# Performance work log

Hardware: AMD Instinct MI355X
Metric: run time of the kernel (lower is better)

Reference implementation:

```python
import math
import jax, jax.numpy as jnp
import numpy as np

HEAD_NUM = 8
DIM = 512
D_K = DIM // HEAD_NUM  # 64
M_FEAT = 256
B, L = 4, 2048
STAB = 1e-5


def _orthogonal_gaussian(m, d, rng):
    num_squares = m // d
    blocks = []
    for _ in range(num_squares):
        q, _ = np.linalg.qr(rng.standard_normal((d, d)))
        blocks.append(q.T)
    rem = m - d * num_squares
    if rem:
        q, _ = np.linalg.qr(rng.standard_normal((d, d)))
        blocks.append(q.T[:rem])
    mat = np.concatenate(blocks, axis=0)
    mat = mat / math.sqrt(num_squares + rem / d)
    return mat.astype(np.float32)


def setup_inputs() -> dict:
    key = jax.random.key(0)
    ks = jax.random.split(key, 12)
    rng = np.random.default_rng(0)
    inp = {
        'query': jax.random.normal(ks[0], (B, L, DIM), jnp.float32),
        'key': jax.random.normal(ks[1], (B, L, DIM), jnp.float32),
        'value': jax.random.normal(ks[2], (B, L, DIM), jnp.float32),
        'proj': jnp.asarray(_orthogonal_gaussian(M_FEAT, D_K, rng)),  # [M, d_k]
        'w_q_w': jax.random.normal(ks[3], (DIM, DIM), jnp.float32) * 0.02,
        'w_q_b': jnp.zeros((DIM,), jnp.float32),
        'w_k_w': jax.random.normal(ks[4], (DIM, DIM), jnp.float32) * 0.02,
        'w_k_b': jnp.zeros((DIM,), jnp.float32),
        'w_v_w': jax.random.normal(ks[5], (DIM, DIM), jnp.float32) * 0.02,
        'w_v_b': jnp.zeros((DIM,), jnp.float32),
        'w_o_w': jax.random.normal(ks[6], (DIM, DIM), jnp.float32) * 0.02,
        'w_o_b': jnp.zeros((DIM,), jnp.float32),
    }
    return inp


def _relu_kernel(data, proj):
    # data: [B,L,H,D], proj: [M,D] -> [B,L,H,M]
    ratio = 1.0 / math.sqrt(proj.shape[0])
    return jax.nn.relu(ratio * jnp.einsum('blhd,md->blhm', data, proj)) + STAB


def _favor_causal(qp, kp, vs):
    # qp, kp: [L,B,H,M]; vs: [L,B,H,D] -> num [L,B,H,D], den [L,B,H]
    b, h, m = qp.shape[1], qp.shape[2], qp.shape[3]
    d = vs.shape[3]
    carry0 = (jnp.zeros((b, h, m, d), qp.dtype), jnp.zeros((b, h, m), qp.dtype))

    def step(carry, inp):
        s_kv, s_k = carry
        q_l, k_l, v_l = inp
        s_kv = s_kv + jnp.einsum('bhm,bhd->bhmd', k_l, v_l)
        s_k = s_k + k_l
        num = jnp.einsum('bhmd,bhm->bhd', s_kv, q_l)
        den = jnp.sum(q_l * s_k, axis=-1)
        return (s_kv, s_k), (num, den)

    _, (num, den) = jax.lax.scan(step, carry0, (qp, kp, vs))
    return num, den


def reference(query, key, value, proj, w_q_w, w_q_b, w_k_w, w_k_b, w_v_w, w_v_b, w_o_w, w_o_b):
    bsz = query.shape[0]
    q = (query @ w_q_w.T + w_q_b).reshape(bsz, -1, HEAD_NUM, D_K)
    k = (key @ w_k_w.T + w_k_b).reshape(bsz, -1, HEAD_NUM, D_K)
    v = (value @ w_v_w.T + w_v_b).reshape(bsz, -1, HEAD_NUM, D_K)
    qp = jnp.swapaxes(_relu_kernel(q, proj), 0, 1)  # [L,B,H,M]
    kp = jnp.swapaxes(_relu_kernel(k, proj), 0, 1)
    vs = jnp.swapaxes(v, 0, 1)                      # [L,B,H,D]
    num, den = _favor_causal(qp, kp, vs)
    attn = jnp.swapaxes(num, 0, 1) / jnp.swapaxes(den, 0, 1)[..., None]  # [B,L,H,D]
    attn = attn.reshape(bsz, -1, HEAD_NUM * D_K)
    return attn @ w_o_w.T + w_o_b
```

## Files before the change

kernel.cpp:

```cpp
#include <hip/hip_runtime.h>
#include <stdint.h>

#define B_ 4
#define L_ 2048
#define H_ 8
#define DK 64
#define M_ 256
#define DIM_ 512
#define NTOK (B_ * L_)
#define CHK 128
#define NC (L_ / CHK)
#define BH (B_ * H_)
#define RATIO 0.0625f
#define STABC 1e-5f

typedef unsigned short ushort_t;
typedef __attribute__((ext_vector_type(8))) short bf8v;
typedef __attribute__((ext_vector_type(4))) float f4v;

#define MFMA16(a, b, c) __builtin_amdgcn_mfma_f32_16x16x32_bf16(a, b, c, 0, 0, 0)

__device__ __forceinline__ ushort_t f2bf(float f) {
  uint32_t u = __float_as_uint(f);
  return (ushort_t)((u + 0x7fffu + ((u >> 16) & 1u)) >> 16);
}
__device__ __forceinline__ float bf2f(ushort_t u) { return __uint_as_float(((uint32_t)u) << 16); }

__device__ __forceinline__ void gll16(const void* g, void* l) {
  __builtin_amdgcn_global_load_lds((const __attribute__((address_space(1))) void*)g,
                                   (__attribute__((address_space(3))) void*)l, 16, 0, 0);
}

__device__ __forceinline__ bf8v ldfrag(const ushort_t* base, int row, int cb) {
  return *(const bf8v*)((const char*)base + row * 128 + (cb ^ ((row & 7) << 4)));
}
__device__ __forceinline__ bf8v ldfrag256(const ushort_t* base, int row, int cb) {
  return *(const bf8v*)((const char*)base + row * 256 + (cb ^ ((row & 7) << 4)));
}
__device__ __forceinline__ bf8v ldfrag512(const ushort_t* base, int row, int cb) {
  return *(const bf8v*)((const char*)base + row * 512 + (cb ^ ((row & 7) << 4)));
}

__global__ __launch_bounds__(256) void cvt_w(const float* __restrict__ wq, const float* __restrict__ wk,
                                             const float* __restrict__ wv, const float* __restrict__ wo,
                                             const float* __restrict__ pj, ushort_t* __restrict__ d) {
  int i = (blockIdx.x * 256 + threadIdx.x) * 8;
  const float* s;
  int off;
  if (i < 262144)       { s = wq; off = i; }
  else if (i < 524288)  { s = wk; off = i - 262144; }
  else if (i < 786432)  { s = wv; off = i - 524288; }
  else if (i < 1048576) { s = wo; off = i - 786432; }
  else                  { s = pj; off = i - 1048576; }
  float4 a = *(const float4*)(s + off);
  float4 b = *(const float4*)(s + off + 4);
  union { ushort_t u[8]; uint4 vv; } o;
  o.u[0] = f2bf(a.x); o.u[1] = f2bf(a.y); o.u[2] = f2bf(a.z); o.u[3] = f2bf(a.w);
  o.u[4] = f2bf(b.x); o.u[5] = f2bf(b.y); o.u[6] = f2bf(b.z); o.u[7] = f2bf(b.w);
  *(uint4*)(d + i) = o.vv;
}

__global__ __launch_bounds__(256) void qkvgemm_k(const float* __restrict__ q, const float* __restrict__ k,
                                                 const float* __restrict__ v, const ushort_t* __restrict__ Wc,
                                                 const float* __restrict__ bq, const float* __restrict__ bk,
                                                 const float* __restrict__ bv, ushort_t* __restrict__ XHq,
                                                 ushort_t* __restrict__ XHk, ushort_t* __restrict__ VT) {
  __shared__ char SB[34816];
  ushort_t* As = (ushort_t*)SB;
  ushort_t* Bs = (ushort_t*)(SB + 16384);
  ushort_t* Tt = (ushort_t*)SB;
  const int z = blockIdx.z;
  const float* X = (z == 0) ? q : (z == 1) ? k : v;
  const ushort_t* Bw = Wc + (size_t)z * 262144;
  const float* bias = (z == 0) ? bq : (z == 1) ? bk : bv;
  const int tid = threadIdx.x, lane = tid & 63, w = tid >> 6;
  const int bm = blockIdx.x * 128, bn = blockIdx.y * 128;
  const int srow = w * 8 + (lane >> 3);
  const int scol = (((lane & 7) * 16) ^ ((lane >> 3) << 4)) >> 1;
  const int wr = (w >> 1) * 64, wc = (w & 1) * 64;
  const int fr = lane & 15, ks = lane >> 4, fq = lane >> 4;
  f4v acc[4][4] = {};
  for (int k0 = 0; k0 < DIM_; k0 += 64) {
#pragma unroll
    for (int i = 0; i < 4; ++i)
      gll16(Bw + (size_t)(bn + i * 32 + srow) * DIM_ + k0 + scol, (char*)Bs + i * 4096 + w * 1024);
#pragma unroll
    for (int i = 0; i < 4; ++i) {
      int e = tid + i * 256;
      int r = e >> 3, g = e & 7;
      const float* src = X + (size_t)(bm + r) * DIM_ + k0 + g * 8;
      float4 f0 = *(const float4*)src;
      float4 f1 = *(const float4*)(src + 4);
      union { ushort_t u[8]; bf8v v8; } pk;
      pk.u[0] = f2bf(f0.x); pk.u[1] = f2bf(f0.y); pk.u[2] = f2bf(f0.z); pk.u[3] = f2bf(f0.w);
      pk.u[4] = f2bf(f1.x); pk.u[5] = f2bf(f1.y); pk.u[6] = f2bf(f1.z); pk.u[7] = f2bf(f1.w);
      *(bf8v*)((char*)As + r * 128 + ((g * 16) ^ ((r & 7) << 4))) = pk.v8;
    }
    __syncthreads();
#pragma unroll
    for (int kk = 0; kk < 2; ++kk) {
      const int cb = kk * 64 + ks * 16;
      bf8v av[4], bv2[4];
#pragma unroll
      for (int m = 0; m < 4; ++m) av[m] = ldfrag(As, wr + m * 16 + fr, cb);
#pragma unroll
      for (int n = 0; n < 4; ++n) bv2[n] = ldfrag(Bs, wc + n * 16 + fr, cb);
#pragma unroll
      for (int m = 0; m < 4; ++m)
#pragma unroll
        for (int n = 0; n < 4; ++n) acc[m][n] = MFMA16(av[m], bv2[n], acc[m][n]);
    }
    __syncthreads();
  }
  if (z == 2) {
#pragma unroll
    for (int m = 0; m < 4; ++m)
#pragma unroll
      for (int n = 0; n < 4; ++n) {
        int cl = wc + n * 16 + fr;
        float bsv = bias[bn + cl];
#pragma unroll
        for (int j = 0; j < 4; ++j) {
          int rl = wr + m * 16 + fq * 4 + j;
          Tt[cl * 136 + rl] = f2bf(acc[m][n][j] + bsv);
        }
      }
    __syncthreads();
    const int dl = tid >> 1, seg = tid & 1;
    const int c = bn + dl;
    const int bh2 = (bm >> 11) * 8 + (c >> 6);
    const int drow = c & 63;
    size_t vbase = ((size_t)(bh2 * 64 + drow)) * L_ + (bm & 2047) + seg * 64;
#pragma unroll
    for (int qq = 0; qq < 8; ++qq)
      *(uint4*)&VT[vbase + qq * 8] = *(const uint4*)&Tt[dl * 136 + seg * 64 + qq * 8];
  } else {
    ushort_t* Y = (z == 0) ? XHq : XHk;
#pragma unroll
    for (int m = 0; m < 4; ++m)
#pragma unroll
      for (int n = 0; n < 4; ++n) {
        int col = bn + wc + n * 16 + fr;
        float bsv = bias[col];
#pragma unroll
        for (int j = 0; j < 4; ++j) {
          int row = bm + wr + m * 16 + fq * 4 + j;
          Y[(size_t)row * DIM_ + col] = f2bf(acc[m][n][j] + bsv);
        }
      }
  }
}

__global__ __launch_bounds__(256) void cp2_k(const ushort_t* __restrict__ XHk, const ushort_t* __restrict__ P,
                                             const ushort_t* __restrict__ VT, ushort_t* __restrict__ kp,
                                             ushort_t* __restrict__ S) {
  __shared__ ushort_t Ps[256 * 64];
  __shared__ ushort_t Xs[128 * 64];
  __shared__ ushort_t Kt[256 * 128];
  const int ci = blockIdx.x, bh = blockIdx.y;
  const int b = bh >> 3, h = bh & 7;
  const int tid = threadIdx.x, lane = tid & 63, w = tid >> 6;
  const int srow = w * 8 + (lane >> 3);
  const int scol = (((lane & 7) * 16) ^ ((lane >> 3) << 4)) >> 1;
  const int fr = lane & 15, ks = lane >> 4, fq = lane >> 4;
  const int l0 = ci * CHK;
#pragma unroll
  for (int i = 0; i < 8; ++i)
    gll16(P + (size_t)(i * 32 + srow) * 64 + scol, (char*)Ps + i * 4096 + w * 1024);
#pragma unroll
  for (int i = 0; i < 4; ++i)
    gll16(XHk + (size_t)(b * L_ + l0 + i * 32 + srow) * DIM_ + h * 64 + scol, (char*)Xs + i * 4096 + w * 1024);
  __syncthreads();
  {
    f4v acc[4][8] = {};
#pragma unroll
    for (int kk = 0; kk < 2; ++kk) {
      const int cb = kk * 64 + ks * 16;
      bf8v av[4], bv[8];
#pragma unroll
      for (int m = 0; m < 4; ++m) av[m] = ldfrag(Ps, w * 64 + m * 16 + fr, cb);
#pragma unroll
      for (int n = 0; n < 8; ++n) bv[n] = ldfrag(Xs, n * 16 + fr, cb);
#pragma unroll
      for (int m = 0; m < 4; ++m)
#pragma unroll
        for (int n = 0; n < 8; ++n) acc[m][n] = MFMA16(av[m], bv[n], acc[m][n]);
    }
#pragma unroll
    for (int m = 0; m < 4; ++m)
#pragma unroll
      for (int n = 0; n < 8; ++n) {
        const int mb = w * 64 + m * 16 + fq * 4;
        const int ll = n * 16 + fr;
        ushort_t bvv[4];
#pragma unroll
        for (int j = 0; j < 4; ++j) {
          float v = fmaxf(RATIO * acc[m][n][j], 0.f) + STABC;
          bvv[j] = f2bf(v);
          *(ushort_t*)((char*)Kt + (mb + j) * 256 + ((ll * 2) ^ (((mb + j) & 7) << 4))) = bvv[j];
        }
        uint2 pk;
        pk.x = (uint32_t)bvv[0] | ((uint32_t)bvv[1] << 16);
        pk.y = (uint32_t)bvv[2] | ((uint32_t)bvv[3] << 16);
        *(uint2*)(kp + ((size_t)bh * L_ + l0 + ll) * M_ + mb) = pk;
      }
  }
  __syncthreads();
  f4v accS[5][4] = {};
  for (int kt = 0; kt < 2; ++kt) {
#pragma unroll
    for (int i = 0; i < 2; ++i)
      gll16(VT + ((size_t)bh * 64 + i * 32 + srow) * L_ + l0 + kt * 64 + scol, (char*)Xs + i * 4096 + w * 1024);
    if (tid < 32) ((uint32_t*)Xs)[2048 + tid] = 0x3f803f80u;
    __syncthreads();
#pragma unroll
    for (int kk = 0; kk < 2; ++kk) {
      const int cbA = kk * 64 + ks * 16;
      const int cbK = kt * 128 + kk * 64 + ks * 16;
      bf8v av[5], bv[4];
#pragma unroll
      for (int a = 0; a < 5; ++a) av[a] = ldfrag(Xs, a * 16 + fr, cbA);
#pragma unroll
      for (int n = 0; n < 4; ++n) bv[n] = ldfrag256(Kt, w * 64 + n * 16 + fr, cbK);
#pragma unroll
      for (int a = 0; a < 5; ++a)
#pragma unroll
        for (int n = 0; n < 4; ++n) accS[a][n] = MFMA16(av[a], bv[n], accS[a][n]);
    }
    __syncthreads();
  }
  const size_t base = ((size_t)bh * NC + ci) * 65;
#pragma unroll
  for (int a = 0; a < 5; ++a)
#pragma unroll
    for (int n = 0; n < 4; ++n)
#pragma unroll
      for (int j = 0; j < 4; ++j) {
        int row = a * 16 + fq * 4 + j;
        if (row < 65) S[(base + row) * M_ + w * 64 + n * 16 + fr] = f2bf(accS[a][n][j]);
      }
}

__global__ __launch_bounds__(256) void prefix2_k(ushort_t* __restrict__ S) {
  const int g = blockIdx.x * 256 + threadIdx.x;
  const int bh = g / 2080, r = g - bh * 2080;
  ushort_t* base = S + (size_t)bh * (NC * 65 * M_) + (size_t)r * 8;
  uint4 v[16];
#pragma unroll
  for (int ci = 0; ci < NC; ++ci) v[ci] = *(const uint4*)(base + (size_t)ci * (65 * M_));
  float c[8] = {};
#pragma unroll
  for (int ci = 0; ci < NC; ++ci) {
    union { uint4 u; ushort_t s[8]; } in, out;
    in.u = v[ci];
#pragma unroll
    for (int e = 0; e < 8; ++e) {
      float t = bf2f(in.s[e]);
      out.s[e] = f2bf(c[e]);
      c[e] += t;
    }
    *(uint4*)(base + (size_t)ci * (65 * M_)) = out.u;
  }
}

__global__ __launch_bounds__(512) void qkout3_k(const ushort_t* __restrict__ XHq, const ushort_t* __restrict__ P,
                                                const ushort_t* __restrict__ kp, const ushort_t* __restrict__ VT,
                                                const ushort_t* __restrict__ S, ushort_t* __restrict__ attn) {
  __shared__ char LB[114688];
  ushort_t* Qp = (ushort_t*)LB;
  ushort_t* R1 = (ushort_t*)(LB + 65536);
  ushort_t* R2 = (ushort_t*)(LB + 98304);
  const int ci = blockIdx.x, bh = blockIdx.y;
  const int b = bh >> 3, h = bh & 7;
  const int tid = threadIdx.x, lane = tid & 63, w = tid >> 6;
  const int srow = w * 8 + (lane >> 3);
  const int scol = (((lane & 7) * 16) ^ ((lane >> 3) << 4)) >> 1;
  const int fr = lane & 15, ks = lane >> 4, fq = lane >> 4;
  const int l0 = ci * CHK;
  const size_t rowb = (size_t)bh * L_ + l0;
  const size_t tokb = (size_t)b * L_ + l0;
  const size_t sbase = ((size_t)bh * NC + ci) * 65;
#pragma unroll
  for (int i = 0; i < 4; ++i)
    gll16(P + (size_t)(i * 64 + srow) * 64 + scol, (char*)R1 + i * 8192 + w * 1024);
#pragma unroll
  for (int i = 0; i < 2; ++i)
    gll16(XHq + (tokb + i * 64 + srow) * DIM_ + h * 64 + scol, (char*)R2 + i * 8192 + w * 1024);
  __syncthreads();
  {
    f4v accF[2][8] = {};
#pragma unroll
    for (int kk = 0; kk < 2; ++kk) {
      const int cb = kk * 64 + ks * 16;
      bf8v av[2], bv[8];
#pragma unroll
      for (int m = 0; m < 2; ++m) av[m] = ldfrag(R1, w * 32 + m * 16 + fr, cb);
#pragma unroll
      for (int n = 0; n < 8; ++n) bv[n] = ldfrag(R2, n * 16 + fr, cb);
#pragma unroll
      for (int m = 0; m < 2; ++m)
#pragma unroll
        for (int n = 0; n < 8; ++n) accF[m][n] = MFMA16(av[m], bv[n], accF[m][n]);
    }
#pragma unroll
    for (int m = 0; m < 2; ++m)
#pragma unroll
      for (int n = 0; n < 8; ++n) {
        const int mb = w * 32 + m * 16 + fq * 4;
        const int ll = n * 16 + fr;
        ushort_t bvv[4];
#pragma unroll
        for (int j = 0; j < 4; ++j)
          bvv[j] = f2bf(fmaxf(RATIO * accF[m][n][j], 0.f) + STABC);
        uint2 pk;
        pk.x = (uint32_t)bvv[0] | ((uint32_t)bvv[1] << 16);
        pk.y = (uint32_t)bvv[2] | ((uint32_t)bvv[3] << 16);
        *(uint2*)((char*)Qp + ll * 512 + ((mb * 2) ^ ((ll & 7) << 4))) = pk;
      }
  }
  __syncthreads();
  const int qr = (w & 3) * 32, qc = (w >> 2) * 64;
  const int orow = w * 16;
  f4v accA[2][4] = {};
  f4v acc2[5] = {};
  for (int kt = 0; kt < 4; ++kt) {
#pragma unroll
    for (int i = 0; i < 2; ++i)
      gll16(kp + (rowb + i * 64 + srow) * M_ + kt * 64 + scol, (char*)R1 + i * 8192 + w * 1024);
    gll16(S + (sbase + srow) * M_ + kt * 64 + scol, (char*)R2 + w * 1024);
    if (tid < 32)
      ((uint32_t*)R2)[2048 + tid] = ((const uint32_t*)(S + (sbase + 64) * M_ + kt * 64))[tid];
    __syncthreads();
#pragma unroll
    for (int kk = 0; kk < 2; ++kk) {
      const int cb = kk * 64 + ks * 16;
      const int cbQ = kt * 128 + cb;
      bf8v aq[2], bk_[4], a2, sv[5];
#pragma unroll
      for (int m = 0; m < 2; ++m) aq[m] = ldfrag512(Qp, qr + m * 16 + fr, cbQ);
#pragma unroll
      for (int n = 0; n < 4; ++n) bk_[n] = ldfrag(R1, qc + n * 16 + fr, cb);
#pragma unroll
      for (int m = 0; m < 2; ++m)
#pragma unroll
        for (int n = 0; n < 4; ++n) accA[m][n] = MFMA16(aq[m], bk_[n], accA[m][n]);
      a2 = ldfrag512(Qp, orow + fr, cbQ);
#pragma unroll
      for (int n = 0; n < 5; ++n) sv[n] = ldfrag(R2, n * 16 + fr, cb);
#pragma unroll
      for (int n = 0; n < 5; ++n) acc2[n] = MFMA16(a2, sv[n], acc2[n]);
    }
    __syncthreads();
  }
#pragma unroll
  for (int m = 0; m < 2; ++m)
#pragma unroll
    for (int n = 0; n < 4; ++n)
#pragma unroll
      for (int j = 0; j < 4; ++j) {
        int row = qr + m * 16 + fq * 4 + j;
        int col = qc + n * 16 + fr;
        float v = (col <= row) ? accA[m][n][j] : 0.f;
        *(ushort_t*)((char*)R1 + row * 256 + ((col * 2) ^ ((row & 7) << 4))) = f2bf(v);
      }
  __syncthreads();
  for (int kt2 = 0; kt2 < 2; ++kt2) {
    gll16(VT + ((size_t)bh * 64 + srow) * L_ + l0 + kt2 * 64 + scol, (char*)R2 + w * 1024);
    if (tid < 32) ((uint32_t*)R2)[2048 + tid] = 0x3f803f80u;
    __syncthreads();
#pragma unroll
    for (int kk = 0; kk < 2; ++kk) {
      const int cb = kk * 64 + ks * 16;
      bf8v a3, sv[5];
      a3 = ldfrag256(R1, orow + fr, kt2 * 128 + cb);
#pragma unroll
      for (int n = 0; n < 5; ++n) sv[n] = ldfrag(R2, n * 16 + fr, cb);
#pragma unroll
      for (int n = 0; n < 5; ++n) acc2[n] = MFMA16(a3, sv[n], acc2[n]);
    }
    __syncthreads();
  }
  float dinv[4];
#pragma unroll
  for (int j = 0; j < 4; ++j) {
    float den = __shfl(acc2[4][j], (lane & 48));
    dinv[j] = 1.f / den;
  }
#pragma unroll
  for (int n = 0; n < 4; ++n)
#pragma unroll
    for (int j = 0; j < 4; ++j) {
      int l = orow + fq * 4 + j;
      int col = h * 64 + n * 16 + fr;
      attn[(tokb + l) * DIM_ + col] = f2bf(acc2[n][j] * dinv[j]);
    }
}

__global__ __launch_bounds__(256) void gemmo_k(const ushort_t* __restrict__ A, const ushort_t* __restrict__ Bw,
                                               const float* __restrict__ bias, float* __restrict__ Y) {
  __shared__ ushort_t As[128 * 64];
  __shared__ ushort_t Bs[128 * 64];
  const int tid = threadIdx.x, lane = tid & 63, w = tid >> 6;
  const int bm = blockIdx.x * 128, bn = blockIdx.y * 128;
  const int srow = w * 8 + (lane >> 3);
  const int scol = (((lane & 7) * 16) ^ ((lane >> 3) << 4)) >> 1;
  const int wr = (w >> 1) * 64, wc = (w & 1) * 64;
  const int fr = lane & 15, ks = lane >> 4, fq = lane >> 4;
  f4v acc[4][4] = {};
  for (int k0 = 0; k0 < DIM_; k0 += 64) {
#pragma unroll
    for (int i = 0; i < 4; ++i) {
      gll16(A + (size_t)(bm + i * 32 + srow) * DIM_ + k0 + scol, (char*)As + i * 4096 + w * 1024);
      gll16(Bw + (size_t)(bn + i * 32 + srow) * DIM_ + k0 + scol, (char*)Bs + i * 4096 + w * 1024);
    }
    __syncthreads();
#pragma unroll
    for (int kk = 0; kk < 2; ++kk) {
      const int cb = kk * 64 + ks * 16;
      bf8v av[4], bv[4];
#pragma unroll
      for (int m = 0; m < 4; ++m) av[m] = ldfrag(As, wr + m * 16 + fr, cb);
#pragma unroll
      for (int n = 0; n < 4; ++n) bv[n] = ldfrag(Bs, wc + n * 16 + fr, cb);
#pragma unroll
      for (int m = 0; m < 4; ++m)
#pragma unroll
        for (int n = 0; n < 4; ++n) acc[m][n] = MFMA16(av[m], bv[n], acc[m][n]);
    }
    __syncthreads();
  }
#pragma unroll
  for (int m = 0; m < 4; ++m)
#pragma unroll
    for (int n = 0; n < 4; ++n) {
      int col = bn + wc + n * 16 + fr;
      float bsv = bias[col];
#pragma unroll
      for (int j = 0; j < 4; ++j) {
        int row = bm + wr + m * 16 + fq * 4 + j;
        Y[(size_t)row * DIM_ + col] = acc[m][n][j] + bsv;
      }
    }
}

extern "C" void kernel_launch(void* const* d_in, const int* in_sizes, int n_in,
                              void* d_out, int out_size, void* d_ws, size_t ws_size,
                              hipStream_t stream) {
  const float* query = (const float*)d_in[0];
  const float* key   = (const float*)d_in[1];
  const float* value = (const float*)d_in[2];
  const float* proj  = (const float*)d_in[3];
  const float* wq = (const float*)d_in[4];
  const float* bq = (const float*)d_in[5];
  const float* wk = (const float*)d_in[6];
  const float* bk = (const float*)d_in[7];
  const float* wv = (const float*)d_in[8];
  const float* bv = (const float*)d_in[9];
  const float* wo = (const float*)d_in[10];
  const float* bo = (const float*)d_in[11];

  char* ws = (char*)d_ws;
  ushort_t* Wc   = (ushort_t*)(ws);
  ushort_t* XHq  = (ushort_t*)(ws + 2129920);
  ushort_t* XHk  = (ushort_t*)(ws + 10518528);
  ushort_t* VT   = (ushort_t*)(ws + 18907136);
  ushort_t* kp   = (ushort_t*)(ws + 27295744);
  ushort_t* Skv  = (ushort_t*)(ws + 60850176);
  ushort_t* attb = (ushort_t*)(ws + 77889536);
  const ushort_t* Wo = Wc + 786432;
  const ushort_t* Pc = Wc + 1048576;

  dim3 blk(256);
  cvt_w<<<520, blk, 0, stream>>>(wq, wk, wv, wo, proj, Wc);
  qkvgemm_k<<<dim3(64, 4, 3), blk, 0, stream>>>(query, key, value, Wc, bq, bk, bv, XHq, XHk, VT);
  cp2_k<<<dim3(NC, BH), blk, 0, stream>>>(XHk, Pc, VT, kp, Skv);
  prefix2_k<<<260, blk, 0, stream>>>(Skv);
  qkout3_k<<<dim3(NC, BH), dim3(512), 0, stream>>>(XHq, Pc, kp, VT, Skv, attb);
  gemmo_k<<<dim3(64, 4), blk, 0, stream>>>(attb, Wo, bo, (float*)d_out);
}
```

Measured before the change: 107.4 us.

## Double-buffer QKV and output GEMMs and halve output GEMM N-tile

The QKV projection GEMM and the output GEMM now use double-buffered shared memory. Each K-step issues loads for the next tile before running the MFMAs on the current one, which hides global-load latency and removes one barrier per iteration. For the QKV GEMM, the fp32 activations are held in registers and converted to bf16 after compute. The output GEMM's N tile shrinks from 128 to 64, doubling its grid to 512 blocks so more CUs are busy. The cost is more LDS per block (64KB for the QKV GEMM), which may reduce occupancy, plus higher register pressure from the prefetched float4 values.

```diff
diff --git a/kernel.cpp b/kernel.cpp
--- a/kernel.cpp
+++ b/kernel.cpp
@@ -65,9 +65,7 @@
                                                  const float* __restrict__ bq, const float* __restrict__ bk,
                                                  const float* __restrict__ bv, ushort_t* __restrict__ XHq,
                                                  ushort_t* __restrict__ XHk, ushort_t* __restrict__ VT) {
-  __shared__ char SB[34816];
-  ushort_t* As = (ushort_t*)SB;
-  ushort_t* Bs = (ushort_t*)(SB + 16384);
+  __shared__ char SB[65536];
   ushort_t* Tt = (ushort_t*)SB;
   const int z = blockIdx.z;
   const float* X = (z == 0) ? q : (z == 1) ? k : v;
@@ -80,35 +78,69 @@
   const int wr = (w >> 1) * 64, wc = (w & 1) * 64;
   const int fr = lane & 15, ks = lane >> 4, fq = lane >> 4;
   f4v acc[4][4] = {};
-  for (int k0 = 0; k0 < DIM_; k0 += 64) {
+  {
 #pragma unroll
     for (int i = 0; i < 4; ++i)
-      gll16(Bw + (size_t)(bn + i * 32 + srow) * DIM_ + k0 + scol, (char*)Bs + i * 4096 + w * 1024);
+      gll16(Bw + (size_t)(bn + i * 32 + srow) * DIM_ + scol, SB + 32768 + i * 4096 + w * 1024);
 #pragma unroll
     for (int i = 0; i < 4; ++i) {
       int e = tid + i * 256;
       int r = e >> 3, g = e & 7;
-      const float* src = X + (size_t)(bm + r) * DIM_ + k0 + g * 8;
+      const float* src = X + (size_t)(bm + r) * DIM_ + g * 8;
       float4 f0 = *(const float4*)src;
       float4 f1 = *(const float4*)(src + 4);
       union { ushort_t u[8]; bf8v v8; } pk;
       pk.u[0] = f2bf(f0.x); pk.u[1] = f2bf(f0.y); pk.u[2] = f2bf(f0.z); pk.u[3] = f2bf(f0.w);
       pk.u[4] = f2bf(f1.x); pk.u[5] = f2bf(f1.y); pk.u[6] = f2bf(f1.z); pk.u[7] = f2bf(f1.w);
-      *(bf8v*)((char*)As + r * 128 + ((g * 16) ^ ((r & 7) << 4))) = pk.v8;
-    }
-    __syncthreads();
+      *(bf8v*)(SB + r * 128 + ((g * 16) ^ ((r & 7) << 4))) = pk.v8;
+    }
+  }
+  __syncthreads();
+  for (int t = 0; t < 8; ++t) {
+    const ushort_t* curA = (const ushort_t*)(SB + (t & 1) * 16384);
+    const ushort_t* curB = (const ushort_t*)(SB + 32768 + (t & 1) * 16384);
+    char* nxtA = SB + ((t + 1) & 1) * 16384;
+    char* nxtB = SB + 32768 + ((t + 1) & 1) * 16384;
+    const int nk = (t + 1) * 64;
+    float4 fA[4][2];
+    if (t < 7) {
+#pragma unroll
+      for (int i = 0; i < 4; ++i) {
+        int e = tid + i * 256;
+        int r = e >> 3, g = e & 7;
+        const float* src = X + (size_t)(bm + r) * DIM_ + nk + g * 8;
+        fA[i][0] = *(const float4*)src;
+        fA[i][1] = *(const float4*)(src + 4);
+      }
+#pragma unroll
+      for (int i = 0; i < 4; ++i)
+        gll16(Bw + (size_t)(bn + i * 32 + srow) * DIM_ + nk + scol, nxtB + i * 4096 + w * 1024);
+    }
 #pragma unroll
     for (int kk = 0; kk < 2; ++kk) {
       const int cb = kk * 64 + ks * 16;
       bf8v av[4], bv2[4];
 #pragma unroll
-      for (int m = 0; m < 4; ++m) av[m] = ldfrag(As, wr + m * 16 + fr, cb);
-#pragma unroll
-      for (int n = 0; n < 4; ++n) bv2[n] = ldfrag(Bs, wc + n * 16 + fr, cb);
+      for (int m = 0; m < 4; ++m) av[m] = ldfrag(curA, wr + m * 16 + fr, cb);
+#pragma unroll
+      for (int n = 0; n < 4; ++n) bv2[n] = ldfrag(curB, wc + n * 16 + fr, cb);
 #pragma unroll
       for (int m = 0; m < 4; ++m)
 #pragma unroll
         for (int n = 0; n < 4; ++n) acc[m][n] = MFMA16(av[m], bv2[n], acc[m][n]);
+    }
+    if (t < 7) {
+#pragma unroll
+      for (int i = 0; i < 4; ++i) {
+        int e = tid + i * 256;
+        int r = e >> 3, g = e & 7;
+        union { ushort_t u[8]; bf8v v8; } pk;
+        pk.u[0] = f2bf(fA[i][0].x); pk.u[1] = f2bf(fA[i][0].y);
+        pk.u[2] = f2bf(fA[i][0].z); pk.u[3] = f2bf(fA[i][0].w);
+        pk.u[4] = f2bf(fA[i][1].x); pk.u[5] = f2bf(fA[i][1].y);
+        pk.u[6] = f2bf(fA[i][1].z); pk.u[7] = f2bf(fA[i][1].w);
+        *(bf8v*)(nxtA + r * 128 + ((g * 16) ^ ((r & 7) << 4))) = pk.v8;
+      }
     }
     __syncthreads();
   }
@@ -398,41 +430,54 @@
 
 __global__ __launch_bounds__(256) void gemmo_k(const ushort_t* __restrict__ A, const ushort_t* __restrict__ Bw,
                                                const float* __restrict__ bias, float* __restrict__ Y) {
-  __shared__ ushort_t As[128 * 64];
-  __shared__ ushort_t Bs[128 * 64];
+  __shared__ char SB[49152];
   const int tid = threadIdx.x, lane = tid & 63, w = tid >> 6;
-  const int bm = blockIdx.x * 128, bn = blockIdx.y * 128;
+  const int bm = blockIdx.x * 128, bn = blockIdx.y * 64;
   const int srow = w * 8 + (lane >> 3);
   const int scol = (((lane & 7) * 16) ^ ((lane >> 3) << 4)) >> 1;
-  const int wr = (w >> 1) * 64, wc = (w & 1) * 64;
+  const int wr = (w >> 1) * 64, wc = (w & 1) * 32;
   const int fr = lane & 15, ks = lane >> 4, fq = lane >> 4;
-  f4v acc[4][4] = {};
-  for (int k0 = 0; k0 < DIM_; k0 += 64) {
-#pragma unroll
-    for (int i = 0; i < 4; ++i) {
-      gll16(A + (size_t)(bm + i * 32 + srow) * DIM_ + k0 + scol, (char*)As + i * 4096 + w * 1024);
-      gll16(Bw + (size_t)(bn + i * 32 + srow) * DIM_ + k0 + scol, (char*)Bs + i * 4096 + w * 1024);
-    }
-    __syncthreads();
+  f4v acc[4][2] = {};
+#pragma unroll
+  for (int i = 0; i < 4; ++i)
+    gll16(A + (size_t)(bm + i * 32 + srow) * DIM_ + scol, SB + i * 4096 + w * 1024);
+#pragma unroll
+  for (int i = 0; i < 2; ++i)
+    gll16(Bw + (size_t)(bn + i * 32 + srow) * DIM_ + scol, SB + 32768 + i * 4096 + w * 1024);
+  __syncthreads();
+  for (int t = 0; t < 8; ++t) {
+    const ushort_t* curA = (const ushort_t*)(SB + (t & 1) * 16384);
+    const ushort_t* curB = (const ushort_t*)(SB + 32768 + (t & 1) * 8192);
+    char* nxtA = SB + ((t + 1) & 1) * 16384;
+    char* nxtB = SB + 32768 + ((t + 1) & 1) * 8192;
+    const int nk = (t + 1) * 64;
+    if (t < 7) {
+#pragma unroll
+      for (int i = 0; i < 4; ++i)
+        gll16(A + (size_t)(bm + i * 32 + srow) * DIM_ + nk + scol, nxtA + i * 4096 + w * 1024);
+#pragma unroll
+      for (int i = 0; i < 2; ++i)
+        gll16(Bw + (size_t)(bn + i * 32 + srow) * DIM_ + nk + scol, nxtB + i * 4096 + w * 1024);
+    }
 #pragma unroll
     for (int kk = 0; kk < 2; ++kk) {
       const int cb = kk * 64 + ks * 16;
-      bf8v av[4], bv[4];
-#pragma unroll
-      for (int m = 0; m < 4; ++m) av[m] = ldfrag(As, wr + m * 16 + fr, cb);
-#pragma unroll
-      for (int n = 0; n < 4; ++n) bv[n] = ldfrag(Bs, wc + n * 16 + fr, cb);
+      bf8v av[4], bv[2];
+#pragma unroll
+      for (int m = 0; m < 4; ++m) av[m] = ldfrag(curA, wr + m * 16 + fr, cb);
+#pragma unroll
+      for (int n = 0; n < 2; ++n) bv[n] = ldfrag(curB, wc + n * 16 + fr, cb);
 #pragma unroll
       for (int m = 0; m < 4; ++m)
 #pragma unroll
-        for (int n = 0; n < 4; ++n) acc[m][n] = MFMA16(av[m], bv[n], acc[m][n]);
+        for (int n = 0; n < 2; ++n) acc[m][n] = MFMA16(av[m], bv[n], acc[m][n]);
     }
     __syncthreads();
   }
 #pragma unroll
   for (int m = 0; m < 4; ++m)
 #pragma unroll
-    for (int n = 0; n < 4; ++n) {
+    for (int n = 0; n < 2; ++n) {
       int col = bn + wc + n * 16 + fr;
       float bsv = bias[col];
 #pragma unroll
@@ -476,5 +521,5 @@
   cp2_k<<<dim3(NC, BH), blk, 0, stream>>>(XHk, Pc, VT, kp, Skv);
   prefix2_k<<<260, blk, 0, stream>>>(Skv);
   qkout3_k<<<dim3(NC, BH), dim3(512), 0, stream>>>(XHq, Pc, kp, VT, Skv, attb);
-  gemmo_k<<<dim3(64, 4), blk, 0, stream>>>(attb, Wo, bo, (float*)d_out);
-}
+  gemmo_k<<<dim3(64, 8), blk, 0, stream>>>(attb, Wo, bo, (float*)d_out);
+}
```

After: 100.3 us. 6.6% less time.
